# Performance work log

Measured on AMD Instinct MI355X. Metric: run time of the kernel, lower is better.

The kernel has to match this reference:

```python
import jax, jax.numpy as jnp
import numpy as np

D_IN = 1024
D_H = 1024

def setup_inputs() -> dict:
    key = jax.random.key(0)
    ks = jax.random.split(key, 9)
    s = 1.0 / np.sqrt(D_IN)
    inp = {
        'x': jax.random.normal(ks[0], (4, 2048, D_IN), dtype=jnp.float32),
        'wq': jax.random.uniform(ks[1], (D_IN, D_H), jnp.float32, -s, s),
        'bq': jax.random.uniform(ks[2], (D_H,), jnp.float32, -s, s),
        'wk': jax.random.uniform(ks[3], (D_IN, D_H), jnp.float32, -s, s),
        'bk': jax.random.uniform(ks[4], (D_H,), jnp.float32, -s, s),
        'wv': jax.random.uniform(ks[5], (D_IN, D_H), jnp.float32, -s, s),
        'bv': jax.random.uniform(ks[6], (D_H,), jnp.float32, -s, s),
        'wo': jax.random.uniform(ks[7], (D_H, D_IN), jnp.float32, -s, s),
        'bo': jax.random.uniform(ks[8], (D_IN,), jnp.float32, -s, s),
    }
    return inp

def reference(x, wq, bq, wk, bk, wv, bv, wo, bo):
    # q,k,v: [b, s, d]
    q = x @ wq + bq
    k = x @ wk + bk
    v = x @ wv + bv
    scale = 1.0 / jnp.sqrt(jnp.asarray(D_H, x.dtype))
    attn = jnp.einsum('bqd,bkd->bqk', q, k) * scale  # [b, s, s]
    attn = jax.nn.softmax(attn, axis=-1)
    score = jnp.einsum('bqk,bkd->bqd', attn, v)
    out = score @ wo + bo
    return out
```

## Files before the change

### kernel.cpp

```cpp
#include <hip/hip_runtime.h>


typedef unsigned short u16;
typedef short bf16x8 __attribute__((ext_vector_type(8)));
typedef float f32x4 __attribute__((ext_vector_type(4)));

#define SEQ 2048
#define DIM 1024

__device__ __forceinline__ u16 f2bf(float f) {
    unsigned u = __builtin_bit_cast(unsigned, f);
    u += 0x7fffu + ((u >> 16) & 1u);
    return (u16)(u >> 16);
}

__device__ __forceinline__ void async16(void* lds, const void* gmem) {
    __builtin_amdgcn_global_load_lds(
        (const __attribute__((address_space(1))) void*)gmem,
        (__attribute__((address_space(3))) void*)lds, 16, 0, 0);
}

#define FENCE() asm volatile("" ::: "memory")

__global__ __launch_bounds__(256) void cast_x_kernel(
    const float* __restrict__ x, u16* __restrict__ xb,
    const float* __restrict__ bq, const float* __restrict__ bk,
    const float* __restrict__ bv, float* __restrict__ bqkv,
    float* __restrict__ l)
{
    const int b = blockIdx.x;
    if (b < 8192) {
        const int idx = b * 256 + threadIdx.x;
        float4 v = ((const float4*)x)[idx];
        ushort4 o;
        o.x = f2bf(v.x); o.y = f2bf(v.y); o.z = f2bf(v.z); o.w = f2bf(v.w);
        ((ushort4*)xb)[idx] = o;
    } else {
        const int i = (b - 8192) * 256 + threadIdx.x;
        if (i < 3072)
            bqkv[i] = (i < 1024) ? bq[i] : (i < 2048) ? bk[i - 1024] : bv[i - 2048];
        else if (i < 3072 + 8192)
            l[i - 3072] = 0.f;
    }
}

__global__ __launch_bounds__(256) void transpose_cast_all(
    const float* __restrict__ W0, const float* __restrict__ W1,
    const float* __restrict__ W2, const float* __restrict__ W3,
    u16* __restrict__ Tqkv, u16* __restrict__ To)
{
    __shared__ float tile[32][33];
    const int z = blockIdx.z;
    const float* W = (z == 0) ? W0 : (z == 1) ? W1 : (z == 2) ? W2 : W3;
    u16* T = (z < 3) ? (Tqkv + (size_t)z * 1048576) : To;

    const int bx = blockIdx.x * 32, by = blockIdx.y * 32;
    const int tx = threadIdx.x, ty = threadIdx.y;
    #pragma unroll
    for (int r = 0; r < 4; ++r)
        tile[ty + r * 8][tx] = W[(size_t)(by + ty + r * 8) * DIM + bx + tx];
    __syncthreads();
    #pragma unroll
    for (int r = 0; r < 4; ++r) {
        const float v = tile[tx][ty + r * 8];
        T[(size_t)(bx + ty + r * 8) * DIM + by + tx] = f2bf(v);
    }
}

#define EPI_BF16BIAS 0
#define EPI_BF16     1
#define EPI_ELOGIT   2
#define EPI_PVOUT    3

template<int EPI, int K, int LDA, int LDB, int LDC>
__global__ __launch_bounds__(256, 2) void gemm4w(
    const u16* __restrict__ A, const u16* __restrict__ Bt,
    const float* __restrict__ bias, u16* __restrict__ C,
    float* __restrict__ Cf, float* __restrict__ lsum,
    float scale, long sA, long sB, long sC)
{
    __shared__ u16 lds[2][2][8192];

    constexpr int NT = K / 64;

    const int z = blockIdx.z;
    const int t = threadIdx.x;
    const int wid = t >> 6, lane = t & 63;
    const int wm = wid >> 1, wn = wid & 1;
    const int lrow = lane & 15, quad = lane >> 4;
    const int m0 = blockIdx.y * 128, n0 = blockIdx.x * 128;

    const int lin = blockIdx.x + gridDim.x * (blockIdx.y + gridDim.y * z);
    const int slot = lin & 3;
    if (slot > 0) __builtin_amdgcn_s_sleep(7);
    if (slot > 1) __builtin_amdgcn_s_sleep(7);
    if (slot > 2) __builtin_amdgcn_s_sleep(7);

    const u16* ABase = A  + (size_t)z * sA + (size_t)m0 * LDA;
    const u16* BBase = Bt + (size_t)z * sB + (size_t)n0 * LDB;

    int srow[4], scolOff[4];
    #pragma unroll
    for (int p = 0; p < 4; ++p) {
        const int s = p * 256 + t, row = s >> 3, c8 = (s & 7) ^ (row & 7);
        srow[p] = row; scolOff[p] = c8 * 8;
    }

    auto stage = [&](int tile, int buf) {
        const int k0 = tile * 64;
        #pragma unroll
        for (int p = 0; p < 4; ++p) {
            const int s = p * 256 + t;
            async16(&lds[buf][0][s * 8],
                    ABase + (size_t)srow[p] * LDA + k0 + scolOff[p]);
        }
        #pragma unroll
        for (int p = 0; p < 4; ++p) {
            const int s = p * 256 + t;
            async16(&lds[buf][1][s * 8],
                    BBase + (size_t)srow[p] * LDB + k0 + scolOff[p]);
        }
    };

    f32x4 acc[4][4];
    #pragma unroll
    for (int i = 0; i < 4; ++i)
        #pragma unroll
        for (int j = 0; j < 4; ++j)
            acc[i][j] = (f32x4){0.f, 0.f, 0.f, 0.f};

    auto ldA1 = [&](int buf, int mi, int ks) -> bf16x8 {
        int b = (wm * 64 + mi * 16 + lrow) * 128 + ks * 64 + quad * 16;
        b ^= ((b >> 7) & 7) << 4;
        return *(const bf16x8*)((const char*)&lds[buf][0][0] + b);
    };
    auto ldB1 = [&](int buf, int ni, int ks) -> bf16x8 {
        int b = (wn * 64 + ni * 16 + lrow) * 128 + ks * 64 + quad * 16;
        b ^= ((b >> 7) & 7) << 4;
        return *(const bf16x8*)((const char*)&lds[buf][1][0] + b);
    };

    stage(0, 0);
    stage(1, 1);

    #pragma unroll 1
    for (int T = 0; T < NT; ++T) {
        const int buf = T & 1;
        if (T + 1 < NT) asm volatile("s_waitcnt vmcnt(8)" ::: "memory");
        else            asm volatile("s_waitcnt vmcnt(0)" ::: "memory");
        __builtin_amdgcn_s_barrier();

        #pragma unroll
        for (int ks = 0; ks < 2; ++ks) {
            bf16x8 aF[4], bF[4];
            #pragma unroll
            for (int mi = 0; mi < 4; ++mi) aF[mi] = ldA1(buf, mi, ks);
            #pragma unroll
            for (int ni = 0; ni < 4; ++ni) bF[ni] = ldB1(buf, ni, ks);
            __builtin_amdgcn_s_setprio(1);
            #pragma unroll
            for (int mi = 0; mi < 4; ++mi)
                #pragma unroll
                for (int ni = 0; ni < 4; ++ni)
                    acc[mi][ni] = __builtin_amdgcn_mfma_f32_16x16x32_bf16(
                        aF[mi], bF[ni], acc[mi][ni], 0, 0, 0);
            __builtin_amdgcn_s_setprio(0);
        }
        FENCE();
        __builtin_amdgcn_s_barrier();
        if (T + 2 < NT) stage(T + 2, buf);
    }

    u16*   Cz  = C  + (size_t)z * sC;
    float* Cfz = Cf ? Cf + (size_t)z * sC : nullptr;

    #pragma unroll
    for (int mi = 0; mi < 4; ++mi) {
        const int row = m0 + wm * 64 + mi * 16 + quad * 4;
        if (EPI == EPI_BF16BIAS) {
            #pragma unroll
            for (int ni = 0; ni < 4; ++ni) {
                const int col = n0 + wn * 64 + ni * 16 + lrow;
                const float bb = bias[col];
                const f32x4 a = acc[mi][ni];
                #pragma unroll
                for (int r = 0; r < 4; ++r)
                    Cz[(size_t)(row + r) * LDC + col] = f2bf(a[r] + bb);
            }
        } else if (EPI == EPI_BF16) {
            #pragma unroll
            for (int ni = 0; ni < 4; ++ni) {
                const int col = n0 + wn * 64 + ni * 16 + lrow;
                const f32x4 a = acc[mi][ni];
                #pragma unroll
                for (int r = 0; r < 4; ++r)
                    Cz[(size_t)(row + r) * LDC + col] = f2bf(a[r]);
            }
        } else if (EPI == EPI_ELOGIT) {
            float rs[4] = {0.f, 0.f, 0.f, 0.f};
            #pragma unroll
            for (int ni = 0; ni < 4; ++ni) {
                const int col = n0 + wn * 64 + ni * 16 + lrow;
                const f32x4 a = acc[mi][ni];
                #pragma unroll
                for (int r = 0; r < 4; ++r) {
                    const float e = __expf(a[r] * scale);
                    Cz[(size_t)(row + r) * LDC + col] = f2bf(e);
                    rs[r] += e;
                }
            }
            #pragma unroll
            for (int r = 0; r < 4; ++r) {
                float s = rs[r];
                s += __shfl_xor(s, 1, 64);
                s += __shfl_xor(s, 2, 64);
                s += __shfl_xor(s, 4, 64);
                s += __shfl_xor(s, 8, 64);
                if (lrow == 0)
                    atomicAdd(&lsum[(size_t)z * 2048 + row + r], s);
            }
        } else {
            float linv[4];
            #pragma unroll
            for (int r = 0; r < 4; ++r)
                linv[r] = 1.0f / lsum[(size_t)z * 2048 + row + r];
            #pragma unroll
            for (int ni = 0; ni < 4; ++ni) {
                const int col = n0 + wn * 64 + ni * 16 + lrow;
                const float bb = bias[col];
                const f32x4 a = acc[mi][ni];
                #pragma unroll
                for (int r = 0; r < 4; ++r)
                    Cfz[(size_t)(row + r) * LDC + col] = a[r] * linv[r] + bb;
            }
        }
    }
}

extern "C" void kernel_launch(void* const* d_in, const int* in_sizes, int n_in,
                              void* d_out, int out_size, void* d_ws, size_t ws_size,
                              hipStream_t stream)
{
    const float* x  = (const float*)d_in[0];
    const float* wq = (const float*)d_in[1];
    const float* bq = (const float*)d_in[2];
    const float* wk = (const float*)d_in[3];
    const float* bk = (const float*)d_in[4];
    const float* wv = (const float*)d_in[5];
    const float* bv = (const float*)d_in[6];
    const float* wo = (const float*)d_in[7];
    const float* bo = (const float*)d_in[8];
    float* out = (float*)d_out;

    u16* w16   = (u16*)d_ws;
    u16* xb    = w16;
    u16* qkv   = w16 + 8388608;
    u16* E     = w16 + 33554432;
    u16* wqkvT = w16 + 50331648;
    u16* woT   = w16 + 53477376;
    float* bqkv = (float*)(w16 + 54525952);
    float* l    = (float*)(w16 + 54532096);
    u16* VWoT  = w16;

    const u16* q_ = qkv;
    const u16* k_ = qkv + 1024;
    const u16* v_ = qkv + 2048;

    cast_x_kernel<<<8236, dim3(256), 0, stream>>>(x, xb, bq, bk, bv, bqkv, l);
    transpose_cast_all<<<dim3(32, 32, 4), dim3(32, 8), 0, stream>>>(
        wq, wk, wv, wo, wqkvT, woT);

    gemm4w<EPI_BF16BIAS, 1024, 1024, 1024, 3072>
        <<<dim3(24, 64, 1), dim3(256), 0, stream>>>(
            xb, wqkvT, bqkv, qkv, nullptr, nullptr, 1.f, 0, 0, 0);

    gemm4w<EPI_ELOGIT, 1024, 3072, 3072, 2048>
        <<<dim3(16, 16, 4), dim3(256), 0, stream>>>(
            q_, k_, nullptr, E, nullptr, l, 0.03125f,
            6291456, 6291456, 4194304);

    gemm4w<EPI_BF16, 1024, 1024, 3072, 2048>
        <<<dim3(16, 8, 4), dim3(256), 0, stream>>>(
            woT, v_, nullptr, VWoT, nullptr, nullptr, 1.f,
            0, 6291456, 2097152);

    gemm4w<EPI_PVOUT, 2048, 2048, 2048, 1024>
        <<<dim3(8, 16, 4), dim3(256), 0, stream>>>(
            E, VWoT, bo, nullptr, out, l, 1.f,
            4194304, 2097152, 2097152);
}
```

Before: 274.1 us.

## Load GEMM B fragments directly from global into registers, bypassing LDS

The B operand is no longer staged through shared memory. Each wave now reads its B MFMA fragments straight from global memory into registers for the next k-tile, and the A operand stays double-buffered in LDS. This halves LDS usage and removes the LDS reads for B. The per-block staggered s_sleep start is also removed. The cost is that B tiles are fetched separately by both waves sharing the same columns, and the register loads are only partly hidden behind the barrier wait.

```diff
diff --git a/kernel.cpp b/kernel.cpp
--- a/kernel.cpp
+++ b/kernel.cpp
@@ -79,7 +79,7 @@
     float* __restrict__ Cf, float* __restrict__ lsum,
     float scale, long sA, long sB, long sC)
 {
-    __shared__ u16 lds[2][2][8192];
+    __shared__ u16 lds[2][8192];
 
     constexpr int NT = K / 64;
 
@@ -90,12 +90,6 @@
     const int lrow = lane & 15, quad = lane >> 4;
     const int m0 = blockIdx.y * 128, n0 = blockIdx.x * 128;
 
-    const int lin = blockIdx.x + gridDim.x * (blockIdx.y + gridDim.y * z);
-    const int slot = lin & 3;
-    if (slot > 0) __builtin_amdgcn_s_sleep(7);
-    if (slot > 1) __builtin_amdgcn_s_sleep(7);
-    if (slot > 2) __builtin_amdgcn_s_sleep(7);
-
     const u16* ABase = A  + (size_t)z * sA + (size_t)m0 * LDA;
     const u16* BBase = Bt + (size_t)z * sB + (size_t)n0 * LDB;
 
@@ -111,15 +105,21 @@
         #pragma unroll
         for (int p = 0; p < 4; ++p) {
             const int s = p * 256 + t;
-            async16(&lds[buf][0][s * 8],
+            async16(&lds[buf][s * 8],
                     ABase + (size_t)srow[p] * LDA + k0 + scolOff[p]);
         }
-        #pragma unroll
-        for (int p = 0; p < 4; ++p) {
-            const int s = p * 256 + t;
-            async16(&lds[buf][1][s * 8],
-                    BBase + (size_t)srow[p] * LDB + k0 + scolOff[p]);
-        }
+    };
+
+    bf16x8 bF[4][2];
+    auto loadB = [&](int tile) {
+        const int k0 = tile * 64;
+        #pragma unroll
+        for (int ni = 0; ni < 4; ++ni)
+            #pragma unroll
+            for (int ks = 0; ks < 2; ++ks)
+                bF[ni][ks] = *(const bf16x8*)(BBase
+                    + (size_t)(wn * 64 + ni * 16 + lrow) * LDB
+                    + k0 + ks * 32 + quad * 8);
     };
 
     f32x4 acc[4][4];
@@ -132,42 +132,39 @@
     auto ldA1 = [&](int buf, int mi, int ks) -> bf16x8 {
         int b = (wm * 64 + mi * 16 + lrow) * 128 + ks * 64 + quad * 16;
         b ^= ((b >> 7) & 7) << 4;
-        return *(const bf16x8*)((const char*)&lds[buf][0][0] + b);
+        return *(const bf16x8*)((const char*)&lds[buf][0] + b);
     };
-    auto ldB1 = [&](int buf, int ni, int ks) -> bf16x8 {
-        int b = (wn * 64 + ni * 16 + lrow) * 128 + ks * 64 + quad * 16;
-        b ^= ((b >> 7) & 7) << 4;
-        return *(const bf16x8*)((const char*)&lds[buf][1][0] + b);
-    };
-
+
+    loadB(0);
+    FENCE();
     stage(0, 0);
     stage(1, 1);
 
     #pragma unroll 1
     for (int T = 0; T < NT; ++T) {
         const int buf = T & 1;
-        if (T + 1 < NT) asm volatile("s_waitcnt vmcnt(8)" ::: "memory");
+        if (T + 1 < NT) asm volatile("s_waitcnt vmcnt(4)" ::: "memory");
         else            asm volatile("s_waitcnt vmcnt(0)" ::: "memory");
         __builtin_amdgcn_s_barrier();
 
         #pragma unroll
         for (int ks = 0; ks < 2; ++ks) {
-            bf16x8 aF[4], bF[4];
+            bf16x8 aF[4];
             #pragma unroll
             for (int mi = 0; mi < 4; ++mi) aF[mi] = ldA1(buf, mi, ks);
-            #pragma unroll
-            for (int ni = 0; ni < 4; ++ni) bF[ni] = ldB1(buf, ni, ks);
             __builtin_amdgcn_s_setprio(1);
             #pragma unroll
             for (int mi = 0; mi < 4; ++mi)
                 #pragma unroll
                 for (int ni = 0; ni < 4; ++ni)
                     acc[mi][ni] = __builtin_amdgcn_mfma_f32_16x16x32_bf16(
-                        aF[mi], bF[ni], acc[mi][ni], 0, 0, 0);
+                        aF[mi], bF[ni][ks], acc[mi][ni], 0, 0, 0);
             __builtin_amdgcn_s_setprio(0);
         }
         FENCE();
         __builtin_amdgcn_s_barrier();
+        if (T + 1 < NT) loadB(T + 1);
+        FENCE();
         if (T + 2 < NT) stage(T + 2, buf);
     }
 
```

After: 404.8 us. 47.7% more time.
